# Kernel tuning notes

Measured on AMD Instinct MI355X. Metric: run time of the kernel, lower is better.

Reference implementation:

```python
import jax, jax.numpy as jnp
import numpy as np

MARGIN = 0.2
BIG = 1e9  # sentinel for masked (positive-pair) entries in the row-min


def setup_inputs() -> dict:
    key = jax.random.key(0)
    k1, k2, k3 = jax.random.split(key, 3)
    B, D, NUM_CLASSES = 4096, 512, 1000
    z_s = jax.random.normal(k1, (B, D), dtype=jnp.float32)
    z_i = jax.random.normal(k2, (B, D), dtype=jnp.float32)
    labels = jax.random.randint(k3, (B,), 0, NUM_CLASSES, dtype=jnp.int64)
    return {"z_s": z_s, "z_i": z_i, "labels": labels}


def reference(z_s, z_i, labels):
    # dists[a, b] = 1 - <z_s[a], z_i[b]>   -- [B, B]
    dists = 1.0 - jnp.einsum("ad,bd->ab", z_s, z_i)
    pos_mask = labels[:, None] == labels[None, :]  # [B, B] same-label pairs

    p = jnp.diagonal(dists)  # positive distance per anchor, [B]
    # hardest negative per anchor: min over entries with different label
    n = jnp.min(jnp.where(pos_mask, BIG, dists), axis=1)  # [B]
    has_neg = ~jnp.all(pos_mask, axis=1)  # anchors with at least one negative

    per_anchor = jax.nn.relu(p - n + MARGIN)  # [B]
    count = jnp.sum(has_neg)
    total = jnp.sum(jnp.where(has_neg, per_anchor, 0.0))
    # mean over anchors that had negatives; 0.0 if none (matches torch fallback)
    return jnp.where(count > 0, total / jnp.maximum(count, 1).astype(total.dtype), 0.0)
```

## Files before the change

kernel.cpp:

```cpp
#include <hip/hip_runtime.h>
#include <hip/hip_bf16.h>

typedef __attribute__((ext_vector_type(8))) short bf16x8;
typedef __attribute__((ext_vector_type(4))) float f32x4;

#define NB 4096
#define ND 512
#define MARGIN_F 0.2f

__device__ __forceinline__ unsigned int enc_f32(float f) {
    unsigned int b = __float_as_uint(f);
    return (b & 0x80000000u) ? ~b : (b | 0x80000000u);
}

__device__ __forceinline__ float dec_f32(unsigned int e) {
    unsigned int b = (e & 0x80000000u) ? (e & 0x7fffffffu) : ~e;
    return __uint_as_float(b);
}

__device__ __forceinline__ void gld_lds16(const void* g, void* l) {
    __builtin_amdgcn_global_load_lds((__attribute__((address_space(1))) void*)g,
                                     (__attribute__((address_space(3))) void*)l,
                                     16, 0, 0);
}

__global__ __launch_bounds__(256) void k_prep(const float* __restrict__ zs,
                                              const float* __restrict__ zi,
                                              __hip_bfloat16* __restrict__ outb,
                                              unsigned int* __restrict__ rowmax) {
    const int bid = blockIdx.x;
    if (bid < 16) rowmax[bid * 256 + threadIdx.x] = 0u;

    int gid = bid * 256 + threadIdx.x;
    int mat = gid >> 18;
    int t   = gid & 0x3FFFF;
    int si  = t >> 6;
    int L   = t & 63;
    const float* src = mat ? zi : zs;
    int row = ((si >> 4) << 4) | (L & 15);
    int col = ((si & 15) << 5) | (((L >> 4) & 3) << 3);
    const float4* p = (const float4*)(src + (size_t)row * ND + col);
    float4 f0 = p[0];
    float4 f1 = p[1];
    union { __hip_bfloat16 h[8]; bf16x8 v; } u;
    u.h[0] = __float2bfloat16(f0.x);
    u.h[1] = __float2bfloat16(f0.y);
    u.h[2] = __float2bfloat16(f0.z);
    u.h[3] = __float2bfloat16(f0.w);
    u.h[4] = __float2bfloat16(f1.x);
    u.h[5] = __float2bfloat16(f1.y);
    u.h[6] = __float2bfloat16(f1.z);
    u.h[7] = __float2bfloat16(f1.w);
    bf16x8* dst = (bf16x8*)(outb + ((size_t)mat << 21) + ((size_t)si << 9) + (L << 3));
    *dst = u.v;
}

__global__ __launch_bounds__(256) void k_gemm_rowmax(const __hip_bfloat16* __restrict__ zsb,
                                                     const __hip_bfloat16* __restrict__ zib,
                                                     const int* __restrict__ labels,
                                                     unsigned int* __restrict__ rowmax,
                                                     float* __restrict__ p_diag) {
    __shared__ __align__(16) unsigned char sA[16384];
    __shared__ __align__(16) unsigned char sB[16384];
    __shared__ int labA[128];
    __shared__ int labB[128];

    const int tid = threadIdx.x;
    const int bx = blockIdx.x, by = blockIdx.y;

    if (tid < 128) labA[tid] = labels[by * 128 + tid];
    else           labB[tid - 128] = labels[bx * 128 + (tid - 128)];

    const char* gA = (const char*)zsb;
    const char* gB = (const char*)zib;
    const int rb0 = tid >> 7;
    const int rem = (tid & 127) << 4;
    size_t aStat[4], bStat[4];
#pragma unroll
    for (int rd = 0; rd < 4; ++rd) {
        int rb = rd * 2 + rb0;
        aStat[rd] = ((size_t)(by * 8 + rb) << 14) + rem;
        bStat[rd] = ((size_t)(bx * 8 + rb) << 14) + rem;
    }

    const int w = tid >> 6, lane = tid & 63;
    const int w_m = w >> 1, w_n = w & 1;
    const int fragOff = lane << 4;

    f32x4 acc[4][4];
#pragma unroll
    for (int i = 0; i < 4; ++i)
#pragma unroll
        for (int j = 0; j < 4; ++j)
            acc[i][j] = (f32x4){0.f, 0.f, 0.f, 0.f};

    for (int ks = 0; ks < 8; ++ks) {
        __syncthreads();
#pragma unroll
        for (int rd = 0; rd < 4; ++rd) {
            gld_lds16(gA + aStat[rd] + (size_t)ks * 2048, sA + rd * 4096 + (tid << 4));
            gld_lds16(gB + bStat[rd] + (size_t)ks * 2048, sB + rd * 4096 + (tid << 4));
        }
        __syncthreads();
#pragma unroll
        for (int kb = 0; kb < 2; ++kb) {
            bf16x8 af[4], bfr[4];
#pragma unroll
            for (int ms = 0; ms < 4; ++ms)
                af[ms] = *(const bf16x8*)(sA + (((w_m * 4 + ms) * 2 + kb) << 10) + fragOff);
#pragma unroll
            for (int ns = 0; ns < 4; ++ns)
                bfr[ns] = *(const bf16x8*)(sB + (((w_n * 4 + ns) * 2 + kb) << 10) + fragOff);
#pragma unroll
            for (int ms = 0; ms < 4; ++ms)
#pragma unroll
                for (int ns = 0; ns < 4; ++ns)
                    acc[ms][ns] = __builtin_amdgcn_mfma_f32_16x16x32_bf16(
                        af[ms], bfr[ns], acc[ms][ns], 0, 0, 0);
        }
    }

    const int quad = lane >> 4;
    const int lcol = lane & 15;

    int lb[4];
#pragma unroll
    for (int ns = 0; ns < 4; ++ns)
        lb[ns] = labB[w_n * 64 + ns * 16 + lcol];

#pragma unroll
    for (int ms = 0; ms < 4; ++ms) {
        int la[4];
#pragma unroll
        for (int r = 0; r < 4; ++r)
            la[r] = labA[w_m * 64 + ms * 16 + quad * 4 + r];
        float mx[4] = {-3.0e38f, -3.0e38f, -3.0e38f, -3.0e38f};
#pragma unroll
        for (int ns = 0; ns < 4; ++ns) {
#pragma unroll
            for (int r = 0; r < 4; ++r) {
                float v = acc[ms][ns][r];
                if (la[r] != lb[ns] && v > mx[r]) mx[r] = v;
            }
        }
#pragma unroll
        for (int r = 0; r < 4; ++r) {
            float m = mx[r];
            m = fmaxf(m, __shfl_xor(m, 1));
            m = fmaxf(m, __shfl_xor(m, 2));
            m = fmaxf(m, __shfl_xor(m, 4));
            m = fmaxf(m, __shfl_xor(m, 8));
            if (lcol == 0 && m > -2.9e38f) {
                int rowg = by * 128 + w_m * 64 + ms * 16 + quad * 4 + r;
                atomicMax(&rowmax[rowg], enc_f32(m));
            }
        }
    }

    if (bx == by && w_m == w_n) {
        int r = lcol - quad * 4;
        if (r >= 0 && r < 4) {
#pragma unroll
            for (int ms = 0; ms < 4; ++ms) {
                int rowg = by * 128 + w_m * 64 + ms * 16 + lcol;
                p_diag[rowg] = 1.0f - acc[ms][ms][r];
            }
        }
    }
}

__global__ __launch_bounds__(1024) void k_finalize(const unsigned int* __restrict__ rowmax,
                                                   const float* __restrict__ p_diag,
                                                   float* __restrict__ out) {
    int tid = threadIdx.x;
    float sum = 0.0f;
    int cnt = 0;
#pragma unroll
    for (int it = 0; it < 4; ++it) {
        int a = tid + it * 1024;
        unsigned int e = rowmax[a];
        if (e != 0u) {
            float n = 1.0f - dec_f32(e);
            float per = p_diag[a] - n + MARGIN_F;
            if (per > 0.0f) sum += per;
            cnt++;
        }
    }
#pragma unroll
    for (int off = 32; off > 0; off >>= 1) {
        sum += __shfl_xor(sum, off);
        cnt += __shfl_xor(cnt, off);
    }
    __shared__ float sSum[16];
    __shared__ int sCnt[16];
    int w = tid >> 6, lane = tid & 63;
    if (lane == 0) { sSum[w] = sum; sCnt[w] = cnt; }
    __syncthreads();
    if (tid == 0) {
        float ts = 0.0f;
        int tc = 0;
#pragma unroll
        for (int i = 0; i < 16; ++i) { ts += sSum[i]; tc += sCnt[i]; }
        out[0] = (tc > 0) ? ts / (float)tc : 0.0f;
    }
}

extern "C" void kernel_launch(void* const* d_in, const int* in_sizes, int n_in,
                              void* d_out, int out_size, void* d_ws, size_t ws_size,
                              hipStream_t stream) {
    (void)in_sizes; (void)n_in; (void)out_size; (void)ws_size;
    const float* zs = (const float*)d_in[0];
    const float* zi = (const float*)d_in[1];
    const int* labels = (const int*)d_in[2];
    float* out = (float*)d_out;

    char* ws = (char*)d_ws;
    __hip_bfloat16* zb = (__hip_bfloat16*)ws;
    unsigned int* rowmax = (unsigned int*)(ws + (8u << 20));
    float* p_diag = (float*)(ws + (8u << 20) + 16384);

    k_prep<<<2048, 256, 0, stream>>>(zs, zi, zb, rowmax);
    dim3 g(32, 32);
    k_gemm_rowmax<<<g, 256, 0, stream>>>(zb, zb + (size_t)NB * ND, labels, rowmax, p_diag);
    k_finalize<<<1, 1024, 0, stream>>>(rowmax, p_diag, out);
}
```

Measured before the change: 104.1 us.

## Switch GEMM to FP8 scaled MFMA with fp8-packed prep layout

Converts the fp32 embeddings to FP8 (e4m3) instead of bf16 in the prep kernel, using a new packed layout that matches the 16x16x128 f8f6f4 scaled MFMA operand format. The GEMM loop drops to four k-steps, and each step issues one scaled MFMA per tile with unit scales instead of two bf16 MFMAs. This halves operand bytes and MFMA instruction count. In exchange, the lower-precision distances risk picking a different hardest negative and failing tolerance.

```diff
diff --git a/kernel.cpp b/kernel.cpp
--- a/kernel.cpp
+++ b/kernel.cpp
@@ -1,12 +1,14 @@
 #include <hip/hip_runtime.h>
 #include <hip/hip_bf16.h>
 
-typedef __attribute__((ext_vector_type(8))) short bf16x8;
+typedef __attribute__((ext_vector_type(8))) int i32x8;
+typedef __attribute__((ext_vector_type(4))) int i32x4;
 typedef __attribute__((ext_vector_type(4))) float f32x4;
 
 #define NB 4096
 #define ND 512
 #define MARGIN_F 0.2f
+#define UNIT_SCALE 0x7F7F7F7F
 
 __device__ __forceinline__ unsigned int enc_f32(float f) {
     unsigned int b = __float_as_uint(f);
@@ -26,37 +28,36 @@
 
 __global__ __launch_bounds__(256) void k_prep(const float* __restrict__ zs,
                                               const float* __restrict__ zi,
-                                              __hip_bfloat16* __restrict__ outb,
+                                              unsigned char* __restrict__ outb,
                                               unsigned int* __restrict__ rowmax) {
     const int bid = blockIdx.x;
     if (bid < 16) rowmax[bid * 256 + threadIdx.x] = 0u;
 
     int gid = bid * 256 + threadIdx.x;
-    int mat = gid >> 18;
-    int t   = gid & 0x3FFFF;
-    int si  = t >> 6;
-    int L   = t & 63;
-    const float* src = mat ? zi : zs;
-    int row = ((si >> 4) << 4) | (L & 15);
-    int col = ((si & 15) << 5) | (((L >> 4) & 3) << 3);
-    const float4* p = (const float4*)(src + (size_t)row * ND + col);
-    float4 f0 = p[0];
-    float4 f1 = p[1];
-    union { __hip_bfloat16 h[8]; bf16x8 v; } u;
-    u.h[0] = __float2bfloat16(f0.x);
-    u.h[1] = __float2bfloat16(f0.y);
-    u.h[2] = __float2bfloat16(f0.z);
-    u.h[3] = __float2bfloat16(f0.w);
-    u.h[4] = __float2bfloat16(f1.x);
-    u.h[5] = __float2bfloat16(f1.y);
-    u.h[6] = __float2bfloat16(f1.z);
-    u.h[7] = __float2bfloat16(f1.w);
-    bf16x8* dst = (bf16x8*)(outb + ((size_t)mat << 21) + ((size_t)si << 9) + (L << 3));
-    *dst = u.v;
-}
-
-__global__ __launch_bounds__(256) void k_gemm_rowmax(const __hip_bfloat16* __restrict__ zsb,
-                                                     const __hip_bfloat16* __restrict__ zib,
+    int mat = gid >> 17;
+    int c   = gid & 0x1FFFF;
+    int si  = c >> 7;
+    int w   = c & 127;
+    int plane = w >> 6, lane = w & 63;
+    int row = ((si >> 2) << 4) | (lane & 15);
+    int kb  = ((si & 3) << 7) | (((lane >> 4) & 3) << 5) | (plane << 4);
+    const float* src = (mat ? zi : zs) + (size_t)row * ND + kb;
+
+    int4 o;
+    int* op = (int*)&o;
+#pragma unroll
+    for (int q = 0; q < 4; ++q) {
+        float4 f = ((const float4*)src)[q];
+        int r = 0;
+        r = __builtin_amdgcn_cvt_pk_fp8_f32(f.x, f.y, r, false);
+        r = __builtin_amdgcn_cvt_pk_fp8_f32(f.z, f.w, r, true);
+        op[q] = r;
+    }
+    *(int4*)(outb + ((size_t)mat << 21) + ((size_t)c << 4)) = o;
+}
+
+__global__ __launch_bounds__(256) void k_gemm_rowmax(const unsigned char* __restrict__ zsb,
+                                                     const unsigned char* __restrict__ zib,
                                                      const int* __restrict__ labels,
                                                      unsigned int* __restrict__ rowmax,
                                                      float* __restrict__ p_diag) {
@@ -79,8 +80,8 @@
 #pragma unroll
     for (int rd = 0; rd < 4; ++rd) {
         int rb = rd * 2 + rb0;
-        aStat[rd] = ((size_t)(by * 8 + rb) << 14) + rem;
-        bStat[rd] = ((size_t)(bx * 8 + rb) << 14) + rem;
+        aStat[rd] = ((size_t)(by * 8 + rb) << 13) + rem;
+        bStat[rd] = ((size_t)(bx * 8 + rb) << 13) + rem;
     }
 
     const int w = tid >> 6, lane = tid & 63;
@@ -94,7 +95,7 @@
         for (int j = 0; j < 4; ++j)
             acc[i][j] = (f32x4){0.f, 0.f, 0.f, 0.f};
 
-    for (int ks = 0; ks < 8; ++ks) {
+    for (int ks = 0; ks < 4; ++ks) {
         __syncthreads();
 #pragma unroll
         for (int rd = 0; rd < 4; ++rd) {
@@ -102,22 +103,31 @@
             gld_lds16(gB + bStat[rd] + (size_t)ks * 2048, sB + rd * 4096 + (tid << 4));
         }
         __syncthreads();
-#pragma unroll
-        for (int kb = 0; kb < 2; ++kb) {
-            bf16x8 af[4], bfr[4];
-#pragma unroll
-            for (int ms = 0; ms < 4; ++ms)
-                af[ms] = *(const bf16x8*)(sA + (((w_m * 4 + ms) * 2 + kb) << 10) + fragOff);
+
+        i32x8 af[4], bfr[4];
+#pragma unroll
+        for (int ms = 0; ms < 4; ++ms) {
+            const unsigned char* base = sA + ((w_m * 4 + ms) << 11) + fragOff;
+            i32x4 lo = *(const i32x4*)base;
+            i32x4 hi = *(const i32x4*)(base + 1024);
+            af[ms] = (i32x8){lo.x, lo.y, lo.z, lo.w, hi.x, hi.y, hi.z, hi.w};
+        }
+#pragma unroll
+        for (int ns = 0; ns < 4; ++ns) {
+            const unsigned char* base = sB + ((w_n * 4 + ns) << 11) + fragOff;
+            i32x4 lo = *(const i32x4*)base;
+            i32x4 hi = *(const i32x4*)(base + 1024);
+            bfr[ns] = (i32x8){lo.x, lo.y, lo.z, lo.w, hi.x, hi.y, hi.z, hi.w};
+        }
+#pragma unroll
+        for (int ms = 0; ms < 4; ++ms)
 #pragma unroll
             for (int ns = 0; ns < 4; ++ns)
-                bfr[ns] = *(const bf16x8*)(sB + (((w_n * 4 + ns) * 2 + kb) << 10) + fragOff);
-#pragma unroll
-            for (int ms = 0; ms < 4; ++ms)
-#pragma unroll
-                for (int ns = 0; ns < 4; ++ns)
-                    acc[ms][ns] = __builtin_amdgcn_mfma_f32_16x16x32_bf16(
-                        af[ms], bfr[ns], acc[ms][ns], 0, 0, 0);
-        }
+                acc[ms][ns] = __builtin_amdgcn_mfma_scale_f32_16x16x128_f8f6f4(
+                    af[ms], bfr[ns], acc[ms][ns],
+                    0, 0,
+                    0, UNIT_SCALE,
+                    0, UNIT_SCALE);
     }
 
     const int quad = lane >> 4;
@@ -215,12 +225,12 @@
     float* out = (float*)d_out;
 
     char* ws = (char*)d_ws;
-    __hip_bfloat16* zb = (__hip_bfloat16*)ws;
-    unsigned int* rowmax = (unsigned int*)(ws + (8u << 20));
-    float* p_diag = (float*)(ws + (8u << 20) + 16384);
-
-    k_prep<<<2048, 256, 0, stream>>>(zs, zi, zb, rowmax);
+    unsigned char* zb = (unsigned char*)ws;
+    unsigned int* rowmax = (unsigned int*)(ws + (4u << 20));
+    float* p_diag = (float*)(ws + (4u << 20) + 16384);
+
+    k_prep<<<1024, 256, 0, stream>>>(zs, zi, zb, rowmax);
     dim3 g(32, 32);
-    k_gemm_rowmax<<<g, 256, 0, stream>>>(zb, zb + (size_t)NB * ND, labels, rowmax, p_diag);
+    k_gemm_rowmax<<<g, 256, 0, stream>>>(zb, zb + (2u << 20), labels, rowmax, p_diag);
     k_finalize<<<1, 1024, 0, stream>>>(rowmax, p_diag, out);
 }
```

Result: slower. 106.8 us (+2.6%).

## Replace global atomicMax row reduction with per-slot partial maxima and multi-block finalize

Applied to the files above, without the earlier changes.

The GEMM kernel no longer does encoded-float atomicMax on a shared per-row buffer. Each (column block, warp-column) pair now writes its row maxima into its own slot of a 64x4096 partial array. The finalize kernel becomes 16 blocks that each reduce 64 partials per row, then combine sums and counts through global atomics and a last-block-done counter. This removes atomic contention in the GEMM epilogue and parallelises the finalize, at the cost of about 1 MB of extra partial writes and reads.

```diff
diff --git a/kernel.cpp b/kernel.cpp
--- a/kernel.cpp
+++ b/kernel.cpp
@@ -7,16 +7,7 @@
 #define NB 4096
 #define ND 512
 #define MARGIN_F 0.2f
-
-__device__ __forceinline__ unsigned int enc_f32(float f) {
-    unsigned int b = __float_as_uint(f);
-    return (b & 0x80000000u) ? ~b : (b | 0x80000000u);
-}
-
-__device__ __forceinline__ float dec_f32(unsigned int e) {
-    unsigned int b = (e & 0x80000000u) ? (e & 0x7fffffffu) : ~e;
-    return __uint_as_float(b);
-}
+#define SENTINEL -3.0e38f
 
 __device__ __forceinline__ void gld_lds16(const void* g, void* l) {
     __builtin_amdgcn_global_load_lds((__attribute__((address_space(1))) void*)g,
@@ -27,9 +18,9 @@
 __global__ __launch_bounds__(256) void k_prep(const float* __restrict__ zs,
                                               const float* __restrict__ zi,
                                               __hip_bfloat16* __restrict__ outb,
-                                              unsigned int* __restrict__ rowmax) {
+                                              unsigned int* __restrict__ ctrl) {
     const int bid = blockIdx.x;
-    if (bid < 16) rowmax[bid * 256 + threadIdx.x] = 0u;
+    if (bid == 16 && threadIdx.x < 3) ctrl[threadIdx.x] = 0u;
 
     int gid = bid * 256 + threadIdx.x;
     int mat = gid >> 18;
@@ -58,7 +49,7 @@
 __global__ __launch_bounds__(256) void k_gemm_rowmax(const __hip_bfloat16* __restrict__ zsb,
                                                      const __hip_bfloat16* __restrict__ zib,
                                                      const int* __restrict__ labels,
-                                                     unsigned int* __restrict__ rowmax,
+                                                     float* __restrict__ partial,
                                                      float* __restrict__ p_diag) {
     __shared__ __align__(16) unsigned char sA[16384];
     __shared__ __align__(16) unsigned char sB[16384];
@@ -128,13 +119,15 @@
     for (int ns = 0; ns < 4; ++ns)
         lb[ns] = labB[w_n * 64 + ns * 16 + lcol];
 
+    float* slot = partial + ((size_t)(bx * 2 + w_n) << 12) + by * 128 + w_m * 64;
+
 #pragma unroll
     for (int ms = 0; ms < 4; ++ms) {
         int la[4];
 #pragma unroll
         for (int r = 0; r < 4; ++r)
             la[r] = labA[w_m * 64 + ms * 16 + quad * 4 + r];
-        float mx[4] = {-3.0e38f, -3.0e38f, -3.0e38f, -3.0e38f};
+        float mx[4] = {SENTINEL, SENTINEL, SENTINEL, SENTINEL};
 #pragma unroll
         for (int ns = 0; ns < 4; ++ns) {
 #pragma unroll
@@ -150,10 +143,8 @@
             m = fmaxf(m, __shfl_xor(m, 2));
             m = fmaxf(m, __shfl_xor(m, 4));
             m = fmaxf(m, __shfl_xor(m, 8));
-            if (lcol == 0 && m > -2.9e38f) {
-                int rowg = by * 128 + w_m * 64 + ms * 16 + quad * 4 + r;
-                atomicMax(&rowmax[rowg], enc_f32(m));
-            }
+            if (lcol == 0)
+                slot[ms * 16 + quad * 4 + r] = m;
         }
     }
 
@@ -169,39 +160,55 @@
     }
 }
 
-__global__ __launch_bounds__(1024) void k_finalize(const unsigned int* __restrict__ rowmax,
-                                                   const float* __restrict__ p_diag,
-                                                   float* __restrict__ out) {
-    int tid = threadIdx.x;
+__global__ __launch_bounds__(256) void k_finalize(const float* __restrict__ partial,
+                                                  const float* __restrict__ p_diag,
+                                                  unsigned int* __restrict__ ctrl,
+                                                  float* __restrict__ out) {
+    const int tid = threadIdx.x;
+    const int a = blockIdx.x * 256 + tid;
+
+    float best = SENTINEL;
+#pragma unroll 8
+    for (int s = 0; s < 64; ++s) {
+        float v = partial[((size_t)s << 12) + a];
+        best = fmaxf(best, v);
+    }
+
     float sum = 0.0f;
     int cnt = 0;
-#pragma unroll
-    for (int it = 0; it < 4; ++it) {
-        int a = tid + it * 1024;
-        unsigned int e = rowmax[a];
-        if (e != 0u) {
-            float n = 1.0f - dec_f32(e);
-            float per = p_diag[a] - n + MARGIN_F;
-            if (per > 0.0f) sum += per;
-            cnt++;
-        }
-    }
+    if (best > -2.9e38f) {
+        float per = p_diag[a] - (1.0f - best) + MARGIN_F;
+        if (per > 0.0f) sum = per;
+        cnt = 1;
+    }
+
 #pragma unroll
     for (int off = 32; off > 0; off >>= 1) {
         sum += __shfl_xor(sum, off);
         cnt += __shfl_xor(cnt, off);
     }
-    __shared__ float sSum[16];
-    __shared__ int sCnt[16];
+    __shared__ float sSum[4];
+    __shared__ int sCnt[4];
     int w = tid >> 6, lane = tid & 63;
     if (lane == 0) { sSum[w] = sum; sCnt[w] = cnt; }
     __syncthreads();
+
+    __shared__ unsigned int sIsLast;
     if (tid == 0) {
-        float ts = 0.0f;
-        int tc = 0;
-#pragma unroll
-        for (int i = 0; i < 16; ++i) { ts += sSum[i]; tc += sCnt[i]; }
-        out[0] = (tc > 0) ? ts / (float)tc : 0.0f;
+        float ts = sSum[0] + sSum[1] + sSum[2] + sSum[3];
+        unsigned int tc = (unsigned int)(sCnt[0] + sCnt[1] + sCnt[2] + sCnt[3]);
+        atomicAdd((float*)&ctrl[1], ts);
+        atomicAdd(&ctrl[2], tc);
+        __threadfence();
+        unsigned int prev = atomicAdd(&ctrl[0], 1u);
+        sIsLast = (prev == 15u) ? 1u : 0u;
+    }
+    __syncthreads();
+    if (sIsLast && tid == 0) {
+        __threadfence();
+        float ts = atomicAdd((float*)&ctrl[1], 0.0f);
+        unsigned int tc = atomicAdd(&ctrl[2], 0u);
+        out[0] = (tc > 0u) ? ts / (float)tc : 0.0f;
     }
 }
 
@@ -216,11 +223,12 @@
 
     char* ws = (char*)d_ws;
     __hip_bfloat16* zb = (__hip_bfloat16*)ws;
-    unsigned int* rowmax = (unsigned int*)(ws + (8u << 20));
-    float* p_diag = (float*)(ws + (8u << 20) + 16384);
-
-    k_prep<<<2048, 256, 0, stream>>>(zs, zi, zb, rowmax);
+    float* partial = (float*)(ws + (8u << 20));
+    float* p_diag = (float*)(ws + (9u << 20));
+    unsigned int* ctrl = (unsigned int*)(ws + (9u << 20) + 16384);
+
+    k_prep<<<2048, 256, 0, stream>>>(zs, zi, zb, ctrl);
     dim3 g(32, 32);
-    k_gemm_rowmax<<<g, 256, 0, stream>>>(zb, zb + (size_t)NB * ND, labels, rowmax, p_diag);
-    k_finalize<<<1, 1024, 0, stream>>>(rowmax, p_diag, out);
-}
+    k_gemm_rowmax<<<g, 256, 0, stream>>>(zb, zb + (size_t)NB * ND, labels, partial, p_diag);
+    k_finalize<<<16, 256, 0, stream>>>(partial, p_diag, ctrl, out);
+}
```

Measured after the change: 112.0 us. +7.6%, slower.
